# Optimization experiments

Hardware: AMD Instinct MI355X
Metric: run time of the kernel (lower is better)

## Reference

```python
import jax, jax.numpy as jnp
import numpy as np

N_NODES = 50000
N_EDGES = 800000
D_IN = 64
D_OUT = 64


def setup_inputs() -> dict:
    key = jax.random.key(0)
    ks = jax.random.split(key, 5)
    feat = jax.random.normal(ks[0], (N_NODES, D_IN), dtype=jnp.float32)
    src = jax.random.randint(ks[1], (N_EDGES,), 0, N_NODES, dtype=jnp.int64)
    dst = jax.random.randint(ks[2], (N_EDGES,), 0, N_NODES, dtype=jnp.int64)
    # Xavier-uniform-ish scale for weights
    lim = float(np.sqrt(6.0 / (D_IN + D_OUT)) * np.sqrt(2.0))
    W_neigh = jax.random.uniform(ks[3], (D_OUT, D_IN), dtype=jnp.float32, minval=-lim, maxval=lim)
    W_self = jax.random.uniform(ks[4], (D_OUT, D_IN), dtype=jnp.float32, minval=-lim, maxval=lim)
    b_self = jnp.zeros((D_OUT,), dtype=jnp.float32)
    return {"feat": feat, "src": src, "dst": dst,
            "W_neigh": W_neigh, "W_self": W_self, "b_self": b_self}


def reference(feat, src, dst, W_neigh, W_self, b_self):
    # srcdata = fc_neigh(feat_src)  -> [N, D_OUT]
    srcdata = feat @ W_neigh.T
    # A_div.T @ srcdata == mean of transformed source feats over in-edges per dst.
    # deg[j] = A.sum(0)[j]; column scaling by 1/deg then transpose-SpMM.
    agg = jax.ops.segment_sum(srcdata[src], dst, num_segments=N_NODES)  # [N, D_OUT]
    deg = jax.ops.segment_sum(jnp.ones_like(dst, dtype=srcdata.dtype), dst,
                              num_segments=N_NODES)  # [N]
    # Zero-degree columns stay zero in the sparse product (no stored nonzeros).
    dstdata = jnp.where(deg[:, None] > 0, agg / jnp.maximum(deg, 1.0)[:, None], 0.0)
    # rst = fc_self(feat_dst) + dstdata ; feat_dst = feat[:N_dst] = feat (square A)
    return feat @ W_self.T + b_self + dstdata
```

## Files before the change

### kernel.cpp

```cpp
#include <hip/hip_runtime.h>

#define N_NODES 50000
#define N_EDGES 800000
#define D 64
#define RB 128
#define NBUCK 391
#define CAP 3072
#define PAD 16
#define NFEATBLK 3125
#define GN 64
#define NCHUNK 196
#define CHUNK 4096
#define ALD 68

typedef __attribute__((ext_vector_type(8))) __bf16 bf16x8;
typedef __attribute__((ext_vector_type(4))) float f32x4;
typedef __attribute__((ext_vector_type(2))) float f32x2;

__device__ inline unsigned f2bf(float f) {
    unsigned b = __builtin_bit_cast(unsigned, f);
    b += 0x7fffu + ((b >> 16) & 1u);
    return b >> 16;
}

__device__ inline void acc16(float* acc, uint4 v) {
    f32x2 a;
    a = __builtin_amdgcn_cvt_pk_f32_fp8((int)v.x, false); acc[0]  += a.x; acc[1]  += a.y;
    a = __builtin_amdgcn_cvt_pk_f32_fp8((int)v.x, true);  acc[2]  += a.x; acc[3]  += a.y;
    a = __builtin_amdgcn_cvt_pk_f32_fp8((int)v.y, false); acc[4]  += a.x; acc[5]  += a.y;
    a = __builtin_amdgcn_cvt_pk_f32_fp8((int)v.y, true);  acc[6]  += a.x; acc[7]  += a.y;
    a = __builtin_amdgcn_cvt_pk_f32_fp8((int)v.z, false); acc[8]  += a.x; acc[9]  += a.y;
    a = __builtin_amdgcn_cvt_pk_f32_fp8((int)v.z, true);  acc[10] += a.x; acc[11] += a.y;
    a = __builtin_amdgcn_cvt_pk_f32_fp8((int)v.w, false); acc[12] += a.x; acc[13] += a.y;
    a = __builtin_amdgcn_cvt_pk_f32_fp8((int)v.w, true);  acc[14] += a.x; acc[15] += a.y;
}

__global__ __launch_bounds__(256) void prep_scatter_kernel(
        const float* __restrict__ feat, const float* __restrict__ Wn, const float* __restrict__ Ws,
        const int* __restrict__ src, const int* __restrict__ dst,
        unsigned* __restrict__ fq,
        unsigned short* __restrict__ wnb, unsigned short* __restrict__ wsb,
        int* __restrict__ bcursor, unsigned int* __restrict__ ebuf) {
    __shared__ int cntB[NBUCK];
    __shared__ int baseB[NBUCK];
    int b = blockIdx.x;
    int t = threadIdx.x;
    if (b < NCHUNK) {
        for (int i = t; i < NBUCK; i += 256) cntB[i] = 0;
        __syncthreads();
        int e0 = b * CHUNK;
        int rec_[16], bk_[16];
#pragma unroll
        for (int k = 0; k < 16; ++k) {
            int e = e0 + k * 256 + t;
            if (e < N_EDGES) {
                int dv = dst[e];
                bk_[k] = dv >> 7;
                rec_[k] = src[e] | ((dv & (RB - 1)) << 16);
                atomicAdd(&cntB[bk_[k]], 1);
            } else bk_[k] = -1;
        }
        __syncthreads();
        for (int i = t; i < NBUCK; i += 256) {
            int c = cntB[i];
            baseB[i] = c ? atomicAdd(&bcursor[i * PAD], c) : 0;
        }
        __syncthreads();
#pragma unroll
        for (int k = 0; k < 16; ++k) {
            if (bk_[k] >= 0) {
                int pos = atomicAdd(&baseB[bk_[k]], 1);
                if (pos < CAP)
                    ebuf[(size_t)bk_[k] * CAP + pos] = (unsigned)rec_[k];
            }
        }
    } else if (b < NCHUNK + NFEATBLK) {
        int i = (b - NCHUNK) * 256 + t;
        float4 v = ((const float4*)feat)[i];
        int q = __builtin_amdgcn_cvt_pk_fp8_f32(v.x, v.y, 0, false);
        q = __builtin_amdgcn_cvt_pk_fp8_f32(v.z, v.w, q, true);
        fq[i] = (unsigned)q;
    } else {
        for (int i = t; i < D * D; i += 256) {
            wnb[i] = (unsigned short)f2bf(Wn[i]);
            wsb[i] = (unsigned short)f2bf(Ws[i]);
        }
    }
}

__global__ __launch_bounds__(256) void gather_mfma_kernel(
        const float* __restrict__ feat, const unsigned char* __restrict__ fq,
        const int* __restrict__ bcursor, const unsigned int* __restrict__ ebuf,
        const unsigned short* __restrict__ wsb, const unsigned short* __restrict__ wnb,
        const float* __restrict__ bias, float* __restrict__ out) {
    __shared__ int cnt[RB];
    __shared__ int cur[RB];
    __shared__ int sorted[CAP];
    __shared__ float agg[GN * ALD];
    int t = threadIdx.x;
    int bk = blockIdx.x >> 1;
    int half = blockIdx.x & 1;
    int s0 = bk * CAP;
    int n = bcursor[bk * PAD];
    if (n > CAP) n = CAP;
    if (t < RB) cnt[t] = 0;
    __syncthreads();
    for (int i = t; i < n; i += 256) atomicAdd(&cnt[ebuf[s0 + i] >> 16], 1);
    __syncthreads();
    int c = (t < RB) ? cnt[t] : 0;
    if (t < RB) cur[t] = c;
    __syncthreads();
    for (int d = 1; d < RB; d <<= 1) {
        int v = (t < RB && t >= d) ? cur[t - d] : 0;
        __syncthreads();
        if (t < RB) cur[t] += v;
        __syncthreads();
    }
    if (t < RB) cur[t] -= c;
    __syncthreads();
    for (int i = t; i < n; i += 256) {
        unsigned r = ebuf[s0 + i];
        int p = atomicAdd(&cur[r >> 16], 1);
        sorted[p] = (int)(r & 0xFFFFu);
    }
    __syncthreads();
    int ns = t >> 2, p = t & 3;
    int dl = half * GN + ns;
    int dg = cnt[dl];
    int start = cur[dl] - dg;
    float acc[16];
#pragma unroll
    for (int j = 0; j < 16; ++j) acc[j] = 0.f;
    const unsigned char* fqp = fq + p * 16;
    int i = 0;
    for (; i + 4 <= dg; i += 4) {
        int id0 = sorted[start + i + 0];
        int id1 = sorted[start + i + 1];
        int id2 = sorted[start + i + 2];
        int id3 = sorted[start + i + 3];
        uint4 v0 = *(const uint4*)(fqp + (size_t)id0 * D);
        uint4 v1 = *(const uint4*)(fqp + (size_t)id1 * D);
        uint4 v2 = *(const uint4*)(fqp + (size_t)id2 * D);
        uint4 v3 = *(const uint4*)(fqp + (size_t)id3 * D);
        acc16(acc, v0); acc16(acc, v1); acc16(acc, v2); acc16(acc, v3);
    }
    for (; i < dg; ++i) {
        int id = sorted[start + i];
        uint4 v = *(const uint4*)(fqp + (size_t)id * D);
        acc16(acc, v);
    }
    float inv = (dg > 0) ? 1.0f / (float)dg : 0.f;
#pragma unroll
    for (int j = 0; j < 16; j += 4) {
        float4 o = make_float4(acc[j] * inv, acc[j + 1] * inv, acc[j + 2] * inv, acc[j + 3] * inv);
        *(float4*)(&agg[ns * ALD + p * 16 + j]) = o;
    }
    __syncthreads();
    int r0 = blockIdx.x * GN;
    int w = t >> 6, lane = t & 63;
    int m = lane & 15, quad = lane >> 4;
    int row = r0 + 16 * w + m;
    int rowA = row < N_NODES ? row : N_NODES - 1;
    const float* fr = feat + (size_t)rowA * D + quad * 8;
    float4 f0 = *(const float4*)(fr + 0);
    float4 f1 = *(const float4*)(fr + 4);
    float4 f2 = *(const float4*)(fr + 32);
    float4 f3 = *(const float4*)(fr + 36);
    bf16x8 aS0, aS1, aA0, aA1;
    aS0[0] = (__bf16)f0.x; aS0[1] = (__bf16)f0.y; aS0[2] = (__bf16)f0.z; aS0[3] = (__bf16)f0.w;
    aS0[4] = (__bf16)f1.x; aS0[5] = (__bf16)f1.y; aS0[6] = (__bf16)f1.z; aS0[7] = (__bf16)f1.w;
    aS1[0] = (__bf16)f2.x; aS1[1] = (__bf16)f2.y; aS1[2] = (__bf16)f2.z; aS1[3] = (__bf16)f2.w;
    aS1[4] = (__bf16)f3.x; aS1[5] = (__bf16)f3.y; aS1[6] = (__bf16)f3.z; aS1[7] = (__bf16)f3.w;
#pragma unroll
    for (int j = 0; j < 8; ++j) {
        aA0[j] = (__bf16)agg[(16 * w + m) * ALD + 0  + quad * 8 + j];
        aA1[j] = (__bf16)agg[(16 * w + m) * ALD + 32 + quad * 8 + j];
    }
#pragma unroll
    for (int tt = 0; tt < 4; ++tt) {
        int nn = 16 * tt + m;
        bf16x8 bS0 = *(const bf16x8*)(wsb + (size_t)nn * D + 0  + quad * 8);
        bf16x8 bS1 = *(const bf16x8*)(wsb + (size_t)nn * D + 32 + quad * 8);
        bf16x8 bN0 = *(const bf16x8*)(wnb + (size_t)nn * D + 0  + quad * 8);
        bf16x8 bN1 = *(const bf16x8*)(wnb + (size_t)nn * D + 32 + quad * 8);
        f32x4 cc = {0.f, 0.f, 0.f, 0.f};
        cc = __builtin_amdgcn_mfma_f32_16x16x32_bf16(aS0, bS0, cc, 0, 0, 0);
        cc = __builtin_amdgcn_mfma_f32_16x16x32_bf16(aS1, bS1, cc, 0, 0, 0);
        cc = __builtin_amdgcn_mfma_f32_16x16x32_bf16(aA0, bN0, cc, 0, 0, 0);
        cc = __builtin_amdgcn_mfma_f32_16x16x32_bf16(aA1, bN1, cc, 0, 0, 0);
        float bv = bias[16 * tt + m];
#pragma unroll
        for (int reg = 0; reg < 4; ++reg) {
            int orow = r0 + 16 * w + quad * 4 + reg;
            if (orow < N_NODES)
                out[(size_t)orow * D + 16 * tt + m] = cc[reg] + bv;
        }
    }
}

extern "C" void kernel_launch(void* const* d_in, const int* in_sizes, int n_in,
                              void* d_out, int out_size, void* d_ws, size_t ws_size,
                              hipStream_t stream) {
    const float* feat  = (const float*)d_in[0];
    const int*   src   = (const int*)d_in[1];
    const int*   dst   = (const int*)d_in[2];
    const float* Wn    = (const float*)d_in[3];
    const float* Wself = (const float*)d_in[4];
    const float* bself = (const float*)d_in[5];
    float* out = (float*)d_out;

    unsigned*       featq = (unsigned*)d_ws;
    unsigned short* wnb   = (unsigned short*)(featq + (size_t)N_NODES * D / 4);
    unsigned short* wsb   = wnb + D * D;
    unsigned int*   ebuf  = (unsigned int*)(wsb + D * D);
    int* bcursor = (int*)(ebuf + (size_t)NBUCK * CAP);

    hipMemsetAsync(bcursor, 0, (size_t)NBUCK * PAD * sizeof(int), stream);

    prep_scatter_kernel<<<NCHUNK + NFEATBLK + 1, 256, 0, stream>>>(
        feat, Wn, Wself, src, dst, featq, wnb, wsb, bcursor, ebuf);
    gather_mfma_kernel<<<2 * NBUCK, 256, 0, stream>>>(
        feat, (const unsigned char*)featq, bcursor, ebuf, wsb, wnb, bself, out);
}
```

Before: 114.2 us.

## Halve scatter chunk size, use packed f32x2 accumulation, unroll gather by eight

The edge-scatter phase now uses 391 chunks of 2048 edges instead of 196 of 4096, which gives more parallel blocks with fewer registers each. The fp8 gather accumulation switches to packed float2 vectors so the compiler can emit packed adds. The gather loop is unrolled to eight outstanding loads to hide more latency. In exchange, more blocks contend on the global bucket-cursor atomics, and the wider unroll raises register pressure.

```diff
diff --git a/kernel.cpp b/kernel.cpp
--- a/kernel.cpp
+++ b/kernel.cpp
@@ -9,8 +9,8 @@
 #define PAD 16
 #define NFEATBLK 3125
 #define GN 64
-#define NCHUNK 196
-#define CHUNK 4096
+#define NCHUNK 391
+#define CHUNK 2048
 #define ALD 68
 
 typedef __attribute__((ext_vector_type(8))) __bf16 bf16x8;
@@ -23,16 +23,15 @@
     return b >> 16;
 }
 
-__device__ inline void acc16(float* acc, uint4 v) {
-    f32x2 a;
-    a = __builtin_amdgcn_cvt_pk_f32_fp8((int)v.x, false); acc[0]  += a.x; acc[1]  += a.y;
-    a = __builtin_amdgcn_cvt_pk_f32_fp8((int)v.x, true);  acc[2]  += a.x; acc[3]  += a.y;
-    a = __builtin_amdgcn_cvt_pk_f32_fp8((int)v.y, false); acc[4]  += a.x; acc[5]  += a.y;
-    a = __builtin_amdgcn_cvt_pk_f32_fp8((int)v.y, true);  acc[6]  += a.x; acc[7]  += a.y;
-    a = __builtin_amdgcn_cvt_pk_f32_fp8((int)v.z, false); acc[8]  += a.x; acc[9]  += a.y;
-    a = __builtin_amdgcn_cvt_pk_f32_fp8((int)v.z, true);  acc[10] += a.x; acc[11] += a.y;
-    a = __builtin_amdgcn_cvt_pk_f32_fp8((int)v.w, false); acc[12] += a.x; acc[13] += a.y;
-    a = __builtin_amdgcn_cvt_pk_f32_fp8((int)v.w, true);  acc[14] += a.x; acc[15] += a.y;
+__device__ inline void acc16p(f32x2* acc, uint4 v) {
+    acc[0] += __builtin_amdgcn_cvt_pk_f32_fp8((int)v.x, false);
+    acc[1] += __builtin_amdgcn_cvt_pk_f32_fp8((int)v.x, true);
+    acc[2] += __builtin_amdgcn_cvt_pk_f32_fp8((int)v.y, false);
+    acc[3] += __builtin_amdgcn_cvt_pk_f32_fp8((int)v.y, true);
+    acc[4] += __builtin_amdgcn_cvt_pk_f32_fp8((int)v.z, false);
+    acc[5] += __builtin_amdgcn_cvt_pk_f32_fp8((int)v.z, true);
+    acc[6] += __builtin_amdgcn_cvt_pk_f32_fp8((int)v.w, false);
+    acc[7] += __builtin_amdgcn_cvt_pk_f32_fp8((int)v.w, true);
 }
 
 __global__ __launch_bounds__(256) void prep_scatter_kernel(
@@ -49,9 +48,9 @@
         for (int i = t; i < NBUCK; i += 256) cntB[i] = 0;
         __syncthreads();
         int e0 = b * CHUNK;
-        int rec_[16], bk_[16];
-#pragma unroll
-        for (int k = 0; k < 16; ++k) {
+        int rec_[8], bk_[8];
+#pragma unroll
+        for (int k = 0; k < 8; ++k) {
             int e = e0 + k * 256 + t;
             if (e < N_EDGES) {
                 int dv = dst[e];
@@ -67,7 +66,7 @@
         }
         __syncthreads();
 #pragma unroll
-        for (int k = 0; k < 16; ++k) {
+        for (int k = 0; k < 8; ++k) {
             if (bk_[k] >= 0) {
                 int pos = atomicAdd(&baseB[bk_[k]], 1);
                 if (pos < CAP)
@@ -128,32 +127,40 @@
     int dl = half * GN + ns;
     int dg = cnt[dl];
     int start = cur[dl] - dg;
-    float acc[16];
-#pragma unroll
-    for (int j = 0; j < 16; ++j) acc[j] = 0.f;
+    f32x2 acc[8];
+#pragma unroll
+    for (int j = 0; j < 8; ++j) acc[j] = (f32x2){0.f, 0.f};
     const unsigned char* fqp = fq + p * 16;
     int i = 0;
+    for (; i + 8 <= dg; i += 8) {
+        int ids[8];
+#pragma unroll
+        for (int j = 0; j < 8; ++j) ids[j] = sorted[start + i + j];
+        uint4 v[8];
+#pragma unroll
+        for (int j = 0; j < 8; ++j) v[j] = *(const uint4*)(fqp + (size_t)ids[j] * D);
+#pragma unroll
+        for (int j = 0; j < 8; ++j) acc16p(acc, v[j]);
+    }
     for (; i + 4 <= dg; i += 4) {
-        int id0 = sorted[start + i + 0];
-        int id1 = sorted[start + i + 1];
-        int id2 = sorted[start + i + 2];
-        int id3 = sorted[start + i + 3];
-        uint4 v0 = *(const uint4*)(fqp + (size_t)id0 * D);
-        uint4 v1 = *(const uint4*)(fqp + (size_t)id1 * D);
-        uint4 v2 = *(const uint4*)(fqp + (size_t)id2 * D);
-        uint4 v3 = *(const uint4*)(fqp + (size_t)id3 * D);
-        acc16(acc, v0); acc16(acc, v1); acc16(acc, v2); acc16(acc, v3);
+        int ids[4];
+#pragma unroll
+        for (int j = 0; j < 4; ++j) ids[j] = sorted[start + i + j];
+        uint4 v[4];
+#pragma unroll
+        for (int j = 0; j < 4; ++j) v[j] = *(const uint4*)(fqp + (size_t)ids[j] * D);
+#pragma unroll
+        for (int j = 0; j < 4; ++j) acc16p(acc, v[j]);
     }
     for (; i < dg; ++i) {
-        int id = sorted[start + i];
-        uint4 v = *(const uint4*)(fqp + (size_t)id * D);
-        acc16(acc, v);
+        uint4 v = *(const uint4*)(fqp + (size_t)sorted[start + i] * D);
+        acc16p(acc, v);
     }
     float inv = (dg > 0) ? 1.0f / (float)dg : 0.f;
 #pragma unroll
-    for (int j = 0; j < 16; j += 4) {
-        float4 o = make_float4(acc[j] * inv, acc[j + 1] * inv, acc[j + 2] * inv, acc[j + 3] * inv);
-        *(float4*)(&agg[ns * ALD + p * 16 + j]) = o;
+    for (int j = 0; j < 8; j += 2) {
+        float4 o = make_float4(acc[j].x * inv, acc[j].y * inv, acc[j + 1].x * inv, acc[j + 1].y * inv);
+        *(float4*)(&agg[ns * ALD + p * 16 + j * 2]) = o;
     }
     __syncthreads();
     int r0 = blockIdx.x * GN;
```

New measurement: 118.8 us. +4.0%, slower.
